# Optimization experiments

Hardware: AMD Instinct MI355X
Metric: run time of the kernel (lower is better)

Reference implementation:

```python
import jax, jax.numpy as jnp
import numpy as np

B, N, D, K = 128, 1000, 196, 48
SIGMA = 0.05


def setup_inputs() -> dict:
    key = jax.random.key(0)
    kx, kn = jax.random.split(key)
    x = jax.random.normal(kx, (B, D), dtype=jnp.float32)
    noise = jax.random.normal(kn, (B, N, D), dtype=jnp.float32)
    return {"x": x, "noise": noise, "sigma": SIGMA}


def reference(x, noise, sigma):
    # x: (b, d); noise: (b, n, d)
    b, d = x.shape
    n = noise.shape[1]
    perturbed = x[:, None, :] + noise * sigma          # (b, n, d)
    _, idx = jax.lax.top_k(perturbed, K)               # (b, n, k) indices into d
    idx = jnp.sort(idx, axis=-1)                       # sorted, as in torch code
    # indicators[b,k,d'] = mean_n one_hot(idx[b,n,k])[d']
    # computed via scatter-add, avoiding the (b,n,k,d) one-hot tensor
    b_idx = jnp.arange(b)[:, None, None]               # (b,1,1)
    k_idx = jnp.arange(K)[None, None, :]               # (1,1,k)
    indicators = jnp.zeros((b, K, d), dtype=x.dtype).at[b_idx, k_idx, idx].add(1.0 / n)
    return indicators
```

## Files before the change

### kernel.cpp

```cpp
#include <hip/hip_runtime.h>


#define BB 128
#define NN 1000
#define DD 196
#define KK 48

constexpr int SPLIT   = 16;
constexpr int THREADS = 256;
constexpr int NWAVES  = THREADS / 64;
constexpr int DH      = DD / 2;
constexpr int LDSN    = KK * DH;

__device__ __forceinline__ int mbcnt64(unsigned long long m) {
  return __builtin_amdgcn_mbcnt_hi((unsigned)(m >> 32),
         __builtin_amdgcn_mbcnt_lo((unsigned)m, 0));
}

template <int CTRL>
__device__ __forceinline__ float dpp_min_step(float v) {
  int t = __builtin_amdgcn_update_dpp(__float_as_int(v), __float_as_int(v),
                                      CTRL, 0xF, 0xF, false);
  return fminf(v, __int_as_float(t));
}
template <int CTRL>
__device__ __forceinline__ float dpp_max_step(float v) {
  int t = __builtin_amdgcn_update_dpp(__float_as_int(v), __float_as_int(v),
                                      CTRL, 0xF, 0xF, false);
  return fmaxf(v, __int_as_float(t));
}

__device__ __forceinline__ float wave_min_f32(float m) {
  m = dpp_min_step<0x111>(m);
  m = dpp_min_step<0x112>(m);
  m = dpp_min_step<0x114>(m);
  m = dpp_min_step<0x118>(m);
  m = dpp_min_step<0x142>(m);
  m = dpp_min_step<0x143>(m);
  return __int_as_float(__builtin_amdgcn_readlane(__float_as_int(m), 63));
}
__device__ __forceinline__ float wave_max_f32(float m) {
  m = dpp_max_step<0x111>(m);
  m = dpp_max_step<0x112>(m);
  m = dpp_max_step<0x114>(m);
  m = dpp_max_step<0x118>(m);
  m = dpp_max_step<0x142>(m);
  m = dpp_max_step<0x143>(m);
  return __int_as_float(__builtin_amdgcn_readlane(__float_as_int(m), 63));
}

__device__ __forceinline__ unsigned key_of(float v) {
  unsigned u = __float_as_uint(v);
  return u ^ (0x80000000u | (unsigned)((int)u >> 31));
}

__global__ __launch_bounds__(64, 4) void pivot_kernel(
    const float* __restrict__ x, float* __restrict__ piv) {
  const int b    = blockIdx.x;
  const int lane = threadIdx.x;
  const bool lv  = lane < 49;
  float4 xv = make_float4(0.f, 0.f, 0.f, 0.f);
  if (lv) xv = *reinterpret_cast<const float4*>(x + b * DD + 4 * lane);
  unsigned xk0 = lv ? key_of(xv.x) : 0u;
  unsigned xk1 = lv ? key_of(xv.y) : 0u;
  unsigned xk2 = lv ? key_of(xv.z) : 0u;
  unsigned xk3 = lv ? key_of(xv.w) : 0u;
  unsigned p = 0u;
  #pragma unroll
  for (int bit = 31; bit >= 0; --bit) {
    unsigned cand = p | (1u << bit);
    int c = __popcll(__ballot(xk0 >= cand)) + __popcll(__ballot(xk1 >= cand))
          + __popcll(__ballot(xk2 >= cand)) + __popcll(__ballot(xk3 >= cand));
    if (c >= KK) p = cand;
  }
  if (lane == 0) {
    unsigned u = (p & 0x80000000u) ? (p ^ 0x80000000u) : ~p;
    piv[b] = __uint_as_float(u);
  }
}

__global__ __launch_bounds__(THREADS, 8) void ptopk_kernel(
    const float* __restrict__ x, const float* __restrict__ noise,
    const float* __restrict__ sigp, const float* __restrict__ pivp,
    float* __restrict__ out) {
  __shared__ unsigned cnt[LDSN];
  const int tid   = threadIdx.x;
  const int b     = blockIdx.x / SPLIT;
  const int split = blockIdx.x % SPLIT;
  const int n0    = (split * NN) / SPLIT;
  const int n1    = ((split + 1) * NN) / SPLIT;

  for (int i = tid; i < LDSN; i += THREADS) cnt[i] = 0u;
  __syncthreads();

  const float sigma = sigp[0];
  const float piv   = pivp[b];
  const int lane = tid & 63;
  const int wv   = tid >> 6;
  const bool lv  = lane < 49;
  const float PINF = __builtin_huge_valf();
  const float NINF = -__builtin_huge_valf();

  float4 xv = make_float4(0.f, 0.f, 0.f, 0.f);
  if (lv) xv = *reinterpret_cast<const float4*>(x + b * DD + 4 * lane);

  const float* nbase = noise + (size_t)b * NN * DD;

  float4 nv = make_float4(0.f, 0.f, 0.f, 0.f);
  if (lv && (n0 + wv) < n1)
    nv = *reinterpret_cast<const float4*>(nbase + (size_t)(n0 + wv) * DD + 4 * lane);

  for (int r = n0 + wv; r < n1; r += NWAVES) {
    const float4 cur = nv;
    if (lv && (r + NWAVES) < n1)
      nv = *reinterpret_cast<const float4*>(nbase + (size_t)(r + NWAVES) * DD + 4 * lane);

    const float v0 = lv ? fmaf(sigma, cur.x, xv.x) : NINF;
    const float v1 = lv ? fmaf(sigma, cur.y, xv.y) : NINF;
    const float v2 = lv ? fmaf(sigma, cur.z, xv.z) : NINF;
    const float v3 = lv ? fmaf(sigma, cur.w, xv.w) : NINF;

    bool s0 = v0 > piv, s1 = v1 > piv, s2 = v2 > piv, s3 = v3 > piv;
    unsigned long long S0 = __ballot(s0), S1 = __ballot(s1),
                       S2 = __ballot(s2), S3 = __ballot(s3);
    const int c = __popcll(S0) + __popcll(S1) + __popcll(S2) + __popcll(S3);

    if (c > KK) {
      int need = c - KK;
      float m0 = s0 ? v0 : PINF, m1 = s1 ? v1 : PINF;
      float m2 = s2 ? v2 : PINF, m3 = s3 ? v3 : PINF;
      for (;;) {
        const float mm = wave_min_f32(fminf(fminf(m0, m1), fminf(m2, m3)));
        const bool e0 = (m0 == mm), e1 = (m1 == mm),
                   e2 = (m2 == mm), e3 = (m3 == mm);
        const unsigned long long E0 = __ballot(e0), E1 = __ballot(e1),
                                 E2 = __ballot(e2), E3 = __ballot(e3);
        const int cv = __popcll(E0) + __popcll(E1) + __popcll(E2) + __popcll(E3);
        if (cv <= need) {
          s0 &= !e0; s1 &= !e1; s2 &= !e2; s3 &= !e3;
          need -= cv;
          if (need == 0) break;
          m0 = e0 ? PINF : m0; m1 = e1 ? PINF : m1;
          m2 = e2 ? PINF : m2; m3 = e3 ? PINF : m3;
        } else {
          const int keep = cv - need;
          int tp = mbcnt64(E0) + mbcnt64(E1) + mbcnt64(E2) + mbcnt64(E3);
          if (e0 && tp >= keep) s0 = false;  tp += e0 ? 1 : 0;
          if (e1 && tp >= keep) s1 = false;  tp += e1 ? 1 : 0;
          if (e2 && tp >= keep) s2 = false;  tp += e2 ? 1 : 0;
          if (e3 && tp >= keep) s3 = false;
          break;
        }
      }
      S0 = __ballot(s0); S1 = __ballot(s1); S2 = __ballot(s2); S3 = __ballot(s3);
    } else if (c < KK) {
      int need = KK - c;
      float m0 = s0 ? NINF : v0, m1 = s1 ? NINF : v1;
      float m2 = s2 ? NINF : v2, m3 = s3 ? NINF : v3;
      for (;;) {
        const float mm = wave_max_f32(fmaxf(fmaxf(m0, m1), fmaxf(m2, m3)));
        const bool e0 = (m0 == mm), e1 = (m1 == mm),
                   e2 = (m2 == mm), e3 = (m3 == mm);
        const unsigned long long E0 = __ballot(e0), E1 = __ballot(e1),
                                 E2 = __ballot(e2), E3 = __ballot(e3);
        const int cv = __popcll(E0) + __popcll(E1) + __popcll(E2) + __popcll(E3);
        if (cv <= need) {
          s0 |= e0; s1 |= e1; s2 |= e2; s3 |= e3;
          need -= cv;
          if (need == 0) break;
          m0 = e0 ? NINF : m0; m1 = e1 ? NINF : m1;
          m2 = e2 ? NINF : m2; m3 = e3 ? NINF : m3;
        } else {
          int tp = mbcnt64(E0) + mbcnt64(E1) + mbcnt64(E2) + mbcnt64(E3);
          if (e0 && tp < need) s0 = true;  tp += e0 ? 1 : 0;
          if (e1 && tp < need) s1 = true;  tp += e1 ? 1 : 0;
          if (e2 && tp < need) s2 = true;  tp += e2 ? 1 : 0;
          if (e3 && tp < need) s3 = true;
          break;
        }
      }
      S0 = __ballot(s0); S1 = __ballot(s1); S2 = __ballot(s2); S3 = __ballot(s3);
    }

    int kp = mbcnt64(S0) + mbcnt64(S1) + mbcnt64(S2) + mbcnt64(S3);
    const int b2 = 2 * lane;
    if (s0) atomicAdd(&cnt[kp * DH + b2],     1u);        kp += s0 ? 1 : 0;
    if (s1) atomicAdd(&cnt[kp * DH + b2],     0x10000u);  kp += s1 ? 1 : 0;
    if (s2) atomicAdd(&cnt[kp * DH + b2 + 1], 1u);        kp += s2 ? 1 : 0;
    if (s3) atomicAdd(&cnt[kp * DH + b2 + 1], 0x10000u);
  }

  __syncthreads();

  const float invn = 1.0f / (float)NN;
  float* ob = out + (size_t)b * KK * DD;
  for (int i = tid; i < LDSN; i += THREADS) {
    const unsigned cv = cnt[i];
    if (cv) {
      const int k   = i / DH;
      const int dd2 = i - k * DH;
      const unsigned lo = cv & 0xFFFFu, hi = cv >> 16;
      float* p = ob + k * DD + 2 * dd2;
      if (lo) atomicAdd(p,     (float)lo * invn);
      if (hi) atomicAdd(p + 1, (float)hi * invn);
    }
  }
}

extern "C" void kernel_launch(void* const* d_in, const int* in_sizes, int n_in,
                              void* d_out, int out_size, void* d_ws, size_t ws_size,
                              hipStream_t stream) {
  (void)in_sizes; (void)n_in; (void)ws_size;
  const float* x     = (const float*)d_in[0];
  const float* noise = (const float*)d_in[1];
  const float* sig   = (const float*)d_in[2];
  float* out = (float*)d_out;
  float* piv = (float*)d_ws;

  (void)hipMemsetAsync(d_out, 0, (size_t)out_size * sizeof(float), stream);
  pivot_kernel<<<dim3(BB), dim3(64), 0, stream>>>(x, piv);
  ptopk_kernel<<<dim3(BB * SPLIT), dim3(THREADS), 0, stream>>>(x, noise, sig, piv, out);
}
```

Measured before the change: 170.0 us.

## Process two noise rows per wave with interleaved selection-fixup reductions

Each wave now handles two noise rows per iteration and runs the min/max fix-up loops for both rows together, interleaving their DPP reduction chains. The upward case is folded into a min-search on negated values, so one unified resolve routine serves both directions. The aim is to hide the latency of the dependent DPP, readlane and ballot steps through instruction-level parallelism, and to double the loads in flight. In exchange, register pressure rises, so the occupancy hint in launch bounds drops from 8 to 6. Tie handling on the negated path relies on lane-order ranking matching the previous code.

```diff
diff --git a/kernel.cpp b/kernel.cpp
--- a/kernel.cpp
+++ b/kernel.cpp
@@ -18,35 +18,55 @@
 }
 
 template <int CTRL>
-__device__ __forceinline__ float dpp_min_step(float v) {
+__device__ __forceinline__ float dppmin(float v) {
   int t = __builtin_amdgcn_update_dpp(__float_as_int(v), __float_as_int(v),
                                       CTRL, 0xF, 0xF, false);
   return fminf(v, __int_as_float(t));
 }
-template <int CTRL>
-__device__ __forceinline__ float dpp_max_step(float v) {
-  int t = __builtin_amdgcn_update_dpp(__float_as_int(v), __float_as_int(v),
-                                      CTRL, 0xF, 0xF, false);
-  return fmaxf(v, __int_as_float(t));
-}
-
-__device__ __forceinline__ float wave_min_f32(float m) {
-  m = dpp_min_step<0x111>(m);
-  m = dpp_min_step<0x112>(m);
-  m = dpp_min_step<0x114>(m);
-  m = dpp_min_step<0x118>(m);
-  m = dpp_min_step<0x142>(m);
-  m = dpp_min_step<0x143>(m);
-  return __int_as_float(__builtin_amdgcn_readlane(__float_as_int(m), 63));
-}
-__device__ __forceinline__ float wave_max_f32(float m) {
-  m = dpp_max_step<0x111>(m);
-  m = dpp_max_step<0x112>(m);
-  m = dpp_max_step<0x114>(m);
-  m = dpp_max_step<0x118>(m);
-  m = dpp_max_step<0x142>(m);
-  m = dpp_max_step<0x143>(m);
-  return __int_as_float(__builtin_amdgcn_readlane(__float_as_int(m), 63));
+
+__device__ __forceinline__ void wave_min2(float a, float b,
+                                          float& mmA, float& mmB) {
+  a = dppmin<0x111>(a); b = dppmin<0x111>(b);
+  a = dppmin<0x112>(a); b = dppmin<0x112>(b);
+  a = dppmin<0x114>(a); b = dppmin<0x114>(b);
+  a = dppmin<0x118>(a); b = dppmin<0x118>(b);
+  a = dppmin<0x142>(a); b = dppmin<0x142>(b);
+  a = dppmin<0x143>(a); b = dppmin<0x143>(b);
+  mmA = __int_as_float(__builtin_amdgcn_readlane(__float_as_int(a), 63));
+  mmB = __int_as_float(__builtin_amdgcn_readlane(__float_as_int(b), 63));
+}
+
+__device__ __forceinline__ void resolve_row(
+    float mm, bool down, int& need,
+    float& w0, float& w1, float& w2, float& w3,
+    bool& s0, bool& s1, bool& s2, bool& s3) {
+  if (!need) return;
+  const bool e0 = (w0 == mm), e1 = (w1 == mm), e2 = (w2 == mm), e3 = (w3 == mm);
+  const unsigned long long E0 = __ballot(e0), E1 = __ballot(e1),
+                           E2 = __ballot(e2), E3 = __ballot(e3);
+  const int cv = __popcll(E0) + __popcll(E1) + __popcll(E2) + __popcll(E3);
+  if (cv <= need) {
+    s0 ^= e0; s1 ^= e1; s2 ^= e2; s3 ^= e3;
+    need -= cv;
+    if (need) {
+      const float PINF = __builtin_huge_valf();
+      w0 = e0 ? PINF : w0; w1 = e1 ? PINF : w1;
+      w2 = e2 ? PINF : w2; w3 = e3 ? PINF : w3;
+    }
+  } else {
+    const int thr = down ? (cv - need) : need;
+    int tp = mbcnt64(E0) + mbcnt64(E1) + mbcnt64(E2) + mbcnt64(E3);
+    bool a0, a1, a2, a3;
+    if (down) {
+      a0 = e0 && tp >= thr; tp += e0; a1 = e1 && tp >= thr; tp += e1;
+      a2 = e2 && tp >= thr; tp += e2; a3 = e3 && tp >= thr;
+    } else {
+      a0 = e0 && tp < thr;  tp += e0; a1 = e1 && tp < thr;  tp += e1;
+      a2 = e2 && tp < thr;  tp += e2; a3 = e3 && tp < thr;
+    }
+    s0 ^= a0; s1 ^= a1; s2 ^= a2; s3 ^= a3;
+    need = 0;
+  }
 }
 
 __device__ __forceinline__ unsigned key_of(float v) {
@@ -79,7 +99,7 @@
   }
 }
 
-__global__ __launch_bounds__(THREADS, 8) void ptopk_kernel(
+__global__ __launch_bounds__(THREADS, 6) void ptopk_kernel(
     const float* __restrict__ x, const float* __restrict__ noise,
     const float* __restrict__ sigp, const float* __restrict__ pivp,
     float* __restrict__ out) {
@@ -106,88 +126,91 @@
 
   const float* nbase = noise + (size_t)b * NN * DD;
 
-  float4 nv = make_float4(0.f, 0.f, 0.f, 0.f);
-  if (lv && (n0 + wv) < n1)
-    nv = *reinterpret_cast<const float4*>(nbase + (size_t)(n0 + wv) * DD + 4 * lane);
-
-  for (int r = n0 + wv; r < n1; r += NWAVES) {
-    const float4 cur = nv;
-    if (lv && (r + NWAVES) < n1)
-      nv = *reinterpret_cast<const float4*>(nbase + (size_t)(r + NWAVES) * DD + 4 * lane);
-
-    const float v0 = lv ? fmaf(sigma, cur.x, xv.x) : NINF;
-    const float v1 = lv ? fmaf(sigma, cur.y, xv.y) : NINF;
-    const float v2 = lv ? fmaf(sigma, cur.z, xv.z) : NINF;
-    const float v3 = lv ? fmaf(sigma, cur.w, xv.w) : NINF;
-
-    bool s0 = v0 > piv, s1 = v1 > piv, s2 = v2 > piv, s3 = v3 > piv;
-    unsigned long long S0 = __ballot(s0), S1 = __ballot(s1),
-                       S2 = __ballot(s2), S3 = __ballot(s3);
-    const int c = __popcll(S0) + __popcll(S1) + __popcll(S2) + __popcll(S3);
-
-    if (c > KK) {
-      int need = c - KK;
-      float m0 = s0 ? v0 : PINF, m1 = s1 ? v1 : PINF;
-      float m2 = s2 ? v2 : PINF, m3 = s3 ? v3 : PINF;
-      for (;;) {
-        const float mm = wave_min_f32(fminf(fminf(m0, m1), fminf(m2, m3)));
-        const bool e0 = (m0 == mm), e1 = (m1 == mm),
-                   e2 = (m2 == mm), e3 = (m3 == mm);
-        const unsigned long long E0 = __ballot(e0), E1 = __ballot(e1),
-                                 E2 = __ballot(e2), E3 = __ballot(e3);
-        const int cv = __popcll(E0) + __popcll(E1) + __popcll(E2) + __popcll(E3);
-        if (cv <= need) {
-          s0 &= !e0; s1 &= !e1; s2 &= !e2; s3 &= !e3;
-          need -= cv;
-          if (need == 0) break;
-          m0 = e0 ? PINF : m0; m1 = e1 ? PINF : m1;
-          m2 = e2 ? PINF : m2; m3 = e3 ? PINF : m3;
-        } else {
-          const int keep = cv - need;
-          int tp = mbcnt64(E0) + mbcnt64(E1) + mbcnt64(E2) + mbcnt64(E3);
-          if (e0 && tp >= keep) s0 = false;  tp += e0 ? 1 : 0;
-          if (e1 && tp >= keep) s1 = false;  tp += e1 ? 1 : 0;
-          if (e2 && tp >= keep) s2 = false;  tp += e2 ? 1 : 0;
-          if (e3 && tp >= keep) s3 = false;
-          break;
-        }
-      }
-      S0 = __ballot(s0); S1 = __ballot(s1); S2 = __ballot(s2); S3 = __ballot(s3);
-    } else if (c < KK) {
-      int need = KK - c;
-      float m0 = s0 ? NINF : v0, m1 = s1 ? NINF : v1;
-      float m2 = s2 ? NINF : v2, m3 = s3 ? NINF : v3;
-      for (;;) {
-        const float mm = wave_max_f32(fmaxf(fmaxf(m0, m1), fmaxf(m2, m3)));
-        const bool e0 = (m0 == mm), e1 = (m1 == mm),
-                   e2 = (m2 == mm), e3 = (m3 == mm);
-        const unsigned long long E0 = __ballot(e0), E1 = __ballot(e1),
-                                 E2 = __ballot(e2), E3 = __ballot(e3);
-        const int cv = __popcll(E0) + __popcll(E1) + __popcll(E2) + __popcll(E3);
-        if (cv <= need) {
-          s0 |= e0; s1 |= e1; s2 |= e2; s3 |= e3;
-          need -= cv;
-          if (need == 0) break;
-          m0 = e0 ? NINF : m0; m1 = e1 ? NINF : m1;
-          m2 = e2 ? NINF : m2; m3 = e3 ? NINF : m3;
-        } else {
-          int tp = mbcnt64(E0) + mbcnt64(E1) + mbcnt64(E2) + mbcnt64(E3);
-          if (e0 && tp < need) s0 = true;  tp += e0 ? 1 : 0;
-          if (e1 && tp < need) s1 = true;  tp += e1 ? 1 : 0;
-          if (e2 && tp < need) s2 = true;  tp += e2 ? 1 : 0;
-          if (e3 && tp < need) s3 = true;
-          break;
-        }
-      }
-      S0 = __ballot(s0); S1 = __ballot(s1); S2 = __ballot(s2); S3 = __ballot(s3);
-    }
-
-    int kp = mbcnt64(S0) + mbcnt64(S1) + mbcnt64(S2) + mbcnt64(S3);
-    const int b2 = 2 * lane;
-    if (s0) atomicAdd(&cnt[kp * DH + b2],     1u);        kp += s0 ? 1 : 0;
-    if (s1) atomicAdd(&cnt[kp * DH + b2],     0x10000u);  kp += s1 ? 1 : 0;
-    if (s2) atomicAdd(&cnt[kp * DH + b2 + 1], 1u);        kp += s2 ? 1 : 0;
-    if (s3) atomicAdd(&cnt[kp * DH + b2 + 1], 0x10000u);
+  float4 nvA = make_float4(0.f, 0.f, 0.f, 0.f);
+  float4 nvB = make_float4(0.f, 0.f, 0.f, 0.f);
+  {
+    const int rA0 = n0 + 2 * wv;
+    if (lv && rA0 < n1)
+      nvA = *reinterpret_cast<const float4*>(nbase + (size_t)rA0 * DD + 4 * lane);
+    if (lv && rA0 + 1 < n1)
+      nvB = *reinterpret_cast<const float4*>(nbase + (size_t)(rA0 + 1) * DD + 4 * lane);
+  }
+
+  for (int rA = n0 + 2 * wv; rA < n1; rA += 2 * NWAVES) {
+    const float4 curA = nvA, curB = nvB;
+    const bool hasB = (rA + 1) < n1;
+    {
+      const int rn = rA + 2 * NWAVES;
+      if (lv && rn < n1)
+        nvA = *reinterpret_cast<const float4*>(nbase + (size_t)rn * DD + 4 * lane);
+      if (lv && rn + 1 < n1)
+        nvB = *reinterpret_cast<const float4*>(nbase + (size_t)(rn + 1) * DD + 4 * lane);
+    }
+
+    const float vA0 = lv ? fmaf(sigma, curA.x, xv.x) : NINF;
+    const float vA1 = lv ? fmaf(sigma, curA.y, xv.y) : NINF;
+    const float vA2 = lv ? fmaf(sigma, curA.z, xv.z) : NINF;
+    const float vA3 = lv ? fmaf(sigma, curA.w, xv.w) : NINF;
+    const bool lvB = lv && hasB;
+    const float vB0 = lvB ? fmaf(sigma, curB.x, xv.x) : NINF;
+    const float vB1 = lvB ? fmaf(sigma, curB.y, xv.y) : NINF;
+    const float vB2 = lvB ? fmaf(sigma, curB.z, xv.z) : NINF;
+    const float vB3 = lvB ? fmaf(sigma, curB.w, xv.w) : NINF;
+
+    bool sA0 = vA0 > piv, sA1 = vA1 > piv, sA2 = vA2 > piv, sA3 = vA3 > piv;
+    bool sB0 = vB0 > piv, sB1 = vB1 > piv, sB2 = vB2 > piv, sB3 = vB3 > piv;
+    const int cA = __popcll(__ballot(sA0)) + __popcll(__ballot(sA1))
+                 + __popcll(__ballot(sA2)) + __popcll(__ballot(sA3));
+    const int cB = __popcll(__ballot(sB0)) + __popcll(__ballot(sB1))
+                 + __popcll(__ballot(sB2)) + __popcll(__ballot(sB3));
+
+    const bool downA = cA >= KK, downB = cB >= KK;
+    int needA = downA ? cA - KK : KK - cA;
+    int needB = hasB ? (downB ? cB - KK : KK - cB) : 0;
+
+    float wA0 = PINF, wA1 = PINF, wA2 = PINF, wA3 = PINF;
+    float wB0 = PINF, wB1 = PINF, wB2 = PINF, wB3 = PINF;
+    if (needA) {
+      if (downA) { wA0 = sA0 ? vA0 : PINF; wA1 = sA1 ? vA1 : PINF;
+                   wA2 = sA2 ? vA2 : PINF; wA3 = sA3 ? vA3 : PINF; }
+      else       { wA0 = sA0 ? PINF : -vA0; wA1 = sA1 ? PINF : -vA1;
+                   wA2 = sA2 ? PINF : -vA2; wA3 = sA3 ? PINF : -vA3; }
+    }
+    if (needB) {
+      if (downB) { wB0 = sB0 ? vB0 : PINF; wB1 = sB1 ? vB1 : PINF;
+                   wB2 = sB2 ? vB2 : PINF; wB3 = sB3 ? vB3 : PINF; }
+      else       { wB0 = sB0 ? PINF : -vB0; wB1 = sB1 ? PINF : -vB1;
+                   wB2 = sB2 ? PINF : -vB2; wB3 = sB3 ? PINF : -vB3; }
+    }
+
+    while (needA | needB) {
+      float mmA, mmB;
+      wave_min2(fminf(fminf(wA0, wA1), fminf(wA2, wA3)),
+                fminf(fminf(wB0, wB1), fminf(wB2, wB3)), mmA, mmB);
+      resolve_row(mmA, downA, needA, wA0, wA1, wA2, wA3, sA0, sA1, sA2, sA3);
+      resolve_row(mmB, downB, needB, wB0, wB1, wB2, wB3, sB0, sB1, sB2, sB3);
+    }
+
+    {
+      const unsigned long long S0 = __ballot(sA0), S1 = __ballot(sA1),
+                               S2 = __ballot(sA2), S3 = __ballot(sA3);
+      int kp = mbcnt64(S0) + mbcnt64(S1) + mbcnt64(S2) + mbcnt64(S3);
+      const int b2 = 2 * lane;
+      if (sA0) atomicAdd(&cnt[kp * DH + b2],     1u);        kp += sA0 ? 1 : 0;
+      if (sA1) atomicAdd(&cnt[kp * DH + b2],     0x10000u);  kp += sA1 ? 1 : 0;
+      if (sA2) atomicAdd(&cnt[kp * DH + b2 + 1], 1u);        kp += sA2 ? 1 : 0;
+      if (sA3) atomicAdd(&cnt[kp * DH + b2 + 1], 0x10000u);
+    }
+    {
+      const unsigned long long S0 = __ballot(sB0), S1 = __ballot(sB1),
+                               S2 = __ballot(sB2), S3 = __ballot(sB3);
+      int kp = mbcnt64(S0) + mbcnt64(S1) + mbcnt64(S2) + mbcnt64(S3);
+      const int b2 = 2 * lane;
+      if (sB0) atomicAdd(&cnt[kp * DH + b2],     1u);        kp += sB0 ? 1 : 0;
+      if (sB1) atomicAdd(&cnt[kp * DH + b2],     0x10000u);  kp += sB1 ? 1 : 0;
+      if (sB2) atomicAdd(&cnt[kp * DH + b2 + 1], 1u);        kp += sB2 ? 1 : 0;
+      if (sB3) atomicAdd(&cnt[kp * DH + b2 + 1], 0x10000u);
+    }
   }
 
   __syncthreads();
```

After: 173.2 us. Within noise of the previous version (+1.9%).
